# Optimization experiments

Measured on AMD Instinct MI355X. Metric: run time of the kernel, lower is better.

The kernel has to match this reference:

```python
import jax, jax.numpy as jnp
import numpy as np

EPS = 1e-20
K, STRIDE, PAD = 5, 2, 2
B, CIN, COUT, H, W = 4, 32, 32, 192, 192
HO = (H + 2 * PAD - K) // STRIDE + 1
WO = (W + 2 * PAD - K) // STRIDE + 1


def _patches(x, pad_value):
    # x: [B,C,H,W] -> [B,C,K*K,HO,WO]; same window layout as F.max_pool2d
    xp = jnp.pad(x, ((0, 0), (0, 0), (PAD, PAD), (PAD, PAD)), constant_values=pad_value)
    cols = [xp[:, :, dy:dy + STRIDE * HO:STRIDE, dx:dx + STRIDE * WO:STRIDE]
            for dy in range(K) for dx in range(K)]
    return jnp.stack(cols, axis=2)


def setup_inputs() -> dict:
    key = jax.random.key(0)
    ks = jax.random.split(key, 9)
    d = jax.random.uniform(ks[0], (B, CIN, H, W), jnp.float32, 0.05, 1.0)
    cd = jax.random.uniform(ks[1], (B, CIN, H, W), jnp.float32)
    s = jax.random.uniform(ks[2], (B, CIN, H, W), jnp.float32)
    cs = jax.random.uniform(ks[3], (B, CIN, H, W), jnp.float32)
    w_s_from_d = jax.random.normal(ks[4], (1, 1, 1, 1), jnp.float32) * 0.5
    w_prop = jax.random.normal(ks[5], (1, CIN, 1, 1), jnp.float32) * 0.5
    spatial_weight = jax.random.normal(ks[6], (CIN, 1, K, K), jnp.float32) * 0.5
    channel_weight = jax.random.normal(ks[7], (COUT, CIN, 1, 1), jnp.float32) * 0.5
    bias = jax.random.normal(ks[8], (1, COUT, 1, 1), jnp.float32) * 0.1
    return {"d": d, "cd": cd, "s": s, "cs": cs, "w_s_from_d": w_s_from_d,
            "w_prop": w_prop, "spatial_weight": spatial_weight,
            "channel_weight": channel_weight, "bias": bias}


def reference(d, cd, s, cs, w_s_from_d, w_prop, spatial_weight, channel_weight, bias):
    # EnforcePos reparameterization applied at forward time
    w_sfd = jax.nn.sigmoid(w_s_from_d)
    w_p = jax.nn.softplus(w_prop)
    sw = jax.nn.softplus(spatial_weight)   # [CIN,1,K,K] depthwise
    cw = jax.nn.softplus(channel_weight)   # [COUT,CIN,1,1]

    # max-pool argmax indices (torch pads with -inf), then gather d/cd at those indices
    j_max = jnp.argmax(_patches(d * cd, -jnp.inf), axis=2, keepdims=True)
    j_min = jnp.argmax(_patches(cd / (d + EPS), -jnp.inf), axis=2, keepdims=True)
    p_d = _patches(d, 0.0)
    p_cd = _patches(cd, 0.0)
    d_max = jnp.take_along_axis(p_d, j_max, axis=2)[:, :, 0]
    d_min = jnp.take_along_axis(p_d, j_min, axis=2)[:, :, 0]
    cd_max = jnp.take_along_axis(p_cd, j_max, axis=2)[:, :, 0]
    cd_min = jnp.take_along_axis(p_cd, j_min, axis=2)[:, :, 0]

    min_div_max = jnp.abs(d_min / (d_max + EPS))
    s_from_d = (1 - w_sfd) * min_div_max + w_sfd * min_div_max ** 2
    cs_from_d = cd_max * cd_min

    # stride > 1: no pre-propagation
    s_prop, cs_prop = s, cs

    dn = ('NCHW', 'OIHW', 'NCHW')
    def dwconv(x):  # depthwise 5x5, stride 2, pad 2
        return jax.lax.conv_general_dilated(
            x, sw, (STRIDE, STRIDE), [(PAD, PAD), (PAD, PAD)],
            feature_group_count=CIN, dimension_numbers=dn)

    nom = dwconv(cs_prop * s_prop)
    denom = dwconv(cs_prop)
    s_spatial = nom / (denom + EPS)
    cs_spatial = denom / (jnp.sum(sw) + EPS)

    cw2 = cw[:, :, 0, 0]  # [COUT,CIN], 1x1 conv == channel mixing
    nom = jnp.einsum('bihw,oi->bohw', cs_spatial * s_spatial, cw2)
    denom = jnp.einsum('bihw,oi->bohw', cs_spatial, cw2)
    s_out = nom / (denom + EPS)
    cs_out = denom / (jnp.sum(cw) + EPS)

    # stride > 1: merge pooled s_from_d afterwards
    s_out = (w_p * cs_out * s_out + cs_from_d * s_from_d) / (w_p * cs_out + cs_from_d + EPS)
    cs_out = (w_p * cs_out + cs_from_d) / (w_p + 1)

    s_out = s_out + bias
    s_out = jax.nn.sigmoid(s_out * 2 - 1) / 2 + 0.5
    return s_out, cs_out / (STRIDE * STRIDE)
```

## Files before the change

### kernel.cpp

```cpp
#include <hip/hip_runtime.h>

#define KK    5
#define PADV  2
#define NB    4
#define NC    32
#define NH    192
#define NW    192
#define NHO   96
#define NWO   96
#define NPX   (NHO * NWO)
#define NPLANE (NB * NC * NPX)
#define EPSF  1e-20f

__device__ __forceinline__ float softplusf(float x) {
    return fmaxf(x, 0.f) + log1pf(expf(-fabsf(x)));
}

#define TROWS 19
#define NJ    98
#define PLD2  100
#define K1T   768

__global__ __launch_bounds__(K1T, 6) void k1(
    const float* __restrict__ dg,
    const float* __restrict__ cdg,
    const float* __restrict__ sg,
    const float* __restrict__ csg,
    const float* __restrict__ wsfdg,
    const float* __restrict__ spwg,
    float* __restrict__ ws)
{
    __shared__ float2 pmv_e[TROWS][PLD2];
    __shared__ float2 pmv_o[TROWS][PLD2];
    __shared__ float2 csss_e[TROWS][PLD2];
    __shared__ float2 csss_o[TROWS][PLD2];
    __shared__ float sw_row[25];
    __shared__ float red[12];
    __shared__ float scal[2];

    const int t  = threadIdx.x;
    const int bx = blockIdx.x;
    const int c  = blockIdx.y;
    const int b  = blockIdx.z;

    float part = 0.f;
    for (int i = t; i < NC * 25; i += K1T) {
        float v = softplusf(spwg[i]);
        part += v;
        int cr = i - c * 25;
        if (cr >= 0 && cr < 25) sw_row[cr] = v;
    }
#pragma unroll
    for (int m = 32; m >= 1; m >>= 1) part += __shfl_xor(part, m, 64);
    if ((t & 63) == 0) red[t >> 6] = part;
    __syncthreads();
    if (t == 0) {
        float acc = 0.f;
#pragma unroll
        for (int i = 0; i < 12; i++) acc += red[i];
        scal[0] = acc;
        scal[1] = 1.f / (1.f + expf(-wsfdg[0]));
    }
    __syncthreads();

    const int gy0 = 16 * bx - 2;
    const size_t base = ((size_t)(b * NC) + c) * (NH * NW);
    const int ITEMS = TROWS * NJ;
#pragma unroll
    for (int it0 = 0; it0 < 3 * K1T; it0 += K1T) {
        const int it = it0 + t;
        if (it < ITEMS) {
            const int r  = it / NJ;
            const int j  = it - r * NJ;
            const int gy = gy0 + r;
            const int cc = 2 * j - 2;
            const bool ok = ((unsigned)gy < NH) && (j >= 1) && (j <= 96);
            float2 dv2 = make_float2(0.f, 0.f), cdv2 = dv2, sv2 = dv2, csv2 = dv2;
            if (ok) {
                const size_t idx = base + (size_t)gy * NW + cc;
                dv2  = *(const float2*)(dg  + idx);
                cdv2 = *(const float2*)(cdg + idx);
                sv2  = *(const float2*)(sg  + idx);
                csv2 = *(const float2*)(csg + idx);
            }
            float2 pe, po, ce, co;
            if (ok) {
                pe = make_float2(dv2.x * cdv2.x, cdv2.x / (dv2.x + EPSF));
                po = make_float2(dv2.y * cdv2.y, cdv2.y / (dv2.y + EPSF));
            } else {
                pe = make_float2(-INFINITY, -INFINITY);
                po = pe;
            }
            ce = make_float2(csv2.x, csv2.x * sv2.x);
            co = make_float2(csv2.y, csv2.y * sv2.y);
            pmv_e[r][j]  = pe;
            pmv_o[r][j]  = po;
            csss_e[r][j] = ce;
            csss_o[r][j] = co;
        }
    }
    __syncthreads();

    const int oyl = t / 96;
    const int ox  = t - oyl * 96;
    const int r0  = oyl * 2;

    float bm = -INFINITY, bv = -INFINITY;
    int   jm = 0, jv = 0;
    float nom = 0.f, den = 0.f;

#pragma unroll
    for (int dy = 0; dy < 5; dy++) {
        const int r = r0 + dy;
        const float w0 = sw_row[dy * 5 + 0];
        const float w1 = sw_row[dy * 5 + 1];
        const float w2 = sw_row[dy * 5 + 2];
        const float w3 = sw_row[dy * 5 + 3];
        const float w4 = sw_row[dy * 5 + 4];

        const float2 e0 = pmv_e[r][ox];
        const float2 o0 = pmv_o[r][ox];
        const float2 e1 = pmv_e[r][ox + 1];
        const float2 o1 = pmv_o[r][ox + 1];
        const float2 e2 = pmv_e[r][ox + 2];

        const float2 c0 = csss_e[r][ox];
        const float2 d1 = csss_o[r][ox];
        const float2 c1 = csss_e[r][ox + 1];
        const float2 d3 = csss_o[r][ox + 1];
        const float2 c2 = csss_e[r][ox + 2];

        if (e0.x > bm) { bm = e0.x; jm = r * 8 + 0; }
        if (e0.y > bv) { bv = e0.y; jv = r * 8 + 0; }
        if (o0.x > bm) { bm = o0.x; jm = r * 8 + 1; }
        if (o0.y > bv) { bv = o0.y; jv = r * 8 + 1; }
        if (e1.x > bm) { bm = e1.x; jm = r * 8 + 2; }
        if (e1.y > bv) { bv = e1.y; jv = r * 8 + 2; }
        if (o1.x > bm) { bm = o1.x; jm = r * 8 + 3; }
        if (o1.y > bv) { bv = o1.y; jv = r * 8 + 3; }
        if (e2.x > bm) { bm = e2.x; jm = r * 8 + 4; }
        if (e2.y > bv) { bv = e2.y; jv = r * 8 + 4; }

        nom += w0 * c0.y; den += w0 * c0.x;
        nom += w1 * d1.y; den += w1 * d1.x;
        nom += w2 * c1.y; den += w2 * c1.x;
        nom += w3 * d3.y; den += w3 * d3.x;
        nom += w4 * c2.y; den += w4 * c2.x;
    }

    const int rm = jm >> 3, dxm = jm & 7;
    const int rv = jv >> 3, dxv = jv & 7;
    const size_t im = base + (size_t)(gy0 + rm) * NW + (2 * ox - 2 + dxm);
    const size_t iv = base + (size_t)(gy0 + rv) * NW + (2 * ox - 2 + dxv);
    const float dmax = dg[im], cdmax = cdg[im];
    const float dmin = dg[iv], cdmin = cdg[iv];

    const float sumsw = scal[0];
    const float wsfd  = scal[1];
    const float mdm  = fabsf(dmin / (dmax + EPSF));
    const float sfd  = (1.f - wsfd) * mdm + wsfd * mdm * mdm;
    const float cfd  = cdmax * cdmin;
    const float ssp  = nom / (den + EPSF);
    const float cssp = den / (sumsw + EPSF);

    const int opx = (8 * bx + oyl) * NWO + ox;
    const size_t oidx = ((size_t)(b * NC) + c) * NPX + opx;
    ws[oidx]                       = cssp * ssp;
    ws[(size_t)NPLANE + oidx]      = cssp;
    ws[2 * (size_t)NPLANE + oidx]  = sfd;
    ws[3 * (size_t)NPLANE + oidx]  = cfd;
}

#define K2PX 32

__global__ __launch_bounds__(256, 8) void k2(
    const float* __restrict__ ws,
    const float* __restrict__ wpropg,
    const float* __restrict__ chwg,
    const float* __restrict__ biasg,
    float* __restrict__ out)
{
    __shared__ float cw_s[NC * NC];
    __shared__ float wp_s[NC];
    __shared__ float bias_s[NC];
    __shared__ float A_s[NC][K2PX + 1];
    __shared__ float B_s[NC][K2PX + 1];
    __shared__ float red[4];
    __shared__ float scal[1];

    const int t    = threadIdx.x;
    const int b    = blockIdx.y;
    const int px0  = blockIdx.x * K2PX;
    const int p    = t & (K2PX - 1);
    const int slot = t >> 5;

    float part = 0.f;
    for (int i = t; i < NC * NC; i += 256) {
        float v = softplusf(chwg[i]); cw_s[i] = v; part += v;
    }
    if (t < NC) { wp_s[t] = softplusf(wpropg[t]); bias_s[t] = biasg[t]; }
#pragma unroll
    for (int m = 32; m >= 1; m >>= 1) part += __shfl_xor(part, m, 64);
    if ((t & 63) == 0) red[t >> 6] = part;
    __syncthreads();
    if (t == 0) scal[0] = red[0] + red[1] + red[2] + red[3];

    const size_t bb = (size_t)b * NC * NPX;
#pragma unroll
    for (int idx = 0; idx < NC * K2PX; idx += 256) {
        const int i  = (idx + t) >> 5;
        const int pp = (idx + t) & (K2PX - 1);
        A_s[i][pp] = ws[bb + (size_t)i * NPX + px0 + pp];
        B_s[i][pp] = ws[(size_t)NPLANE + bb + (size_t)i * NPX + px0 + pp];
    }
    __syncthreads();

    const float sumcw = scal[0];
    const int px = px0 + p;

    float nom2[4], den2[4];
#pragma unroll
    for (int k = 0; k < 4; k++) { nom2[k] = 0.f; den2[k] = 0.f; }

#pragma unroll
    for (int i = 0; i < NC; i++) {
        const float a  = A_s[i][p];
        const float b2 = B_s[i][p];
#pragma unroll
        for (int k = 0; k < 4; k++) {
            const float w = cw_s[(slot + 8 * k) * NC + i];
            nom2[k] += w * a;
            den2[k] += w * b2;
        }
    }

#pragma unroll
    for (int k = 0; k < 4; k++) {
        const int o = slot + 8 * k;
        const size_t oidx = bb + (size_t)o * NPX + px;
        const float sfd = ws[2 * (size_t)NPLANE + oidx];
        const float cfd = ws[3 * (size_t)NPLANE + oidx];

        const float smix  = nom2[k] / (den2[k] + EPSF);
        const float csmix = den2[k] / (sumcw + EPSF);
        const float wp    = wp_s[o];

        float sout = (wp * csmix * smix + cfd * sfd) / (wp * csmix + cfd + EPSF);
        const float csout = (wp * csmix + cfd) / (wp + 1.f);

        sout += bias_s[o];
        sout = 1.f / (1.f + expf(-(sout * 2.f - 1.f))) * 0.5f + 0.5f;

        out[oidx]                  = sout;
        out[(size_t)NPLANE + oidx] = csout * 0.25f;
    }
}

#define TW    8
#define TH    4
#define TPP   33

__global__ __launch_bounds__(256, 4) void fused_kernel(
    const float* __restrict__ dg,
    const float* __restrict__ cdg,
    const float* __restrict__ sg,
    const float* __restrict__ csg,
    const float* __restrict__ wsfdg,
    const float* __restrict__ wpropg,
    const float* __restrict__ spwg,
    const float* __restrict__ chwg,
    const float* __restrict__ biasg,
    float* __restrict__ out)
{
    __shared__ float sw_s[NC * 25];
    __shared__ float cw_s[NC * NC];
    __shared__ float wp_s[NC];
    __shared__ float bias_s[NC];
    __shared__ float A_s[NC][TPP];
    __shared__ float B_s[NC][TPP];
    __shared__ float S_s[NC][TPP];
    __shared__ float C_s[NC][TPP];
    __shared__ float red[8];
    __shared__ float scal[3];

    const int t = threadIdx.x;
    const int b = blockIdx.z;
    const int tile_x = blockIdx.x * TW;
    const int tile_y = blockIdx.y * TH;

    float p_sw = 0.f, p_cw = 0.f;
    for (int i = t; i < NC * 25; i += 256) { float v = softplusf(spwg[i]); sw_s[i] = v; p_sw += v; }
    for (int i = t; i < NC * NC; i += 256) { float v = softplusf(chwg[i]); cw_s[i] = v; p_cw += v; }
    if (t < NC) { wp_s[t] = softplusf(wpropg[t]); bias_s[t] = biasg[t]; }
#pragma unroll
    for (int m = 32; m >= 1; m >>= 1) {
        p_sw += __shfl_xor(p_sw, m, 64);
        p_cw += __shfl_xor(p_cw, m, 64);
    }
    if ((t & 63) == 0) { red[(t >> 6) * 2] = p_sw; red[(t >> 6) * 2 + 1] = p_cw; }
    __syncthreads();
    if (t == 0) {
        scal[0] = red[0] + red[2] + red[4] + red[6];
        scal[1] = red[1] + red[3] + red[5] + red[7];
        scal[2] = 1.f / (1.f + expf(-wsfdg[0]));
    }
    __syncthreads();

    const float sumsw = scal[0];
    const float sumcw = scal[1];
    const float wsfd  = scal[2];

    const int c  = t >> 3;
    const int tr = (t >> 2) & 1;
    const int q  = t & 3;
    const int oy0 = tile_y + tr * 2;
    const int ox0 = tile_x + q * 2;
    const int cb = ox0 * 2 - 2;
    const int rb = oy0 * 2 - 2;
    const size_t base = ((size_t)(b * NC) + c) * NH * NW;
    const float* __restrict__ dp  = dg  + base;
    const float* __restrict__ cdp = cdg + base;
    const float* __restrict__ sp  = sg  + base;
    const float* __restrict__ csp = csg + base;

    bool slotok[4];
#pragma unroll
    for (int k = 0; k < 4; k++) slotok[k] = (cb + 2 * k >= 0) && (cb + 2 * k + 1 < NW);
    bool ciok[7];
#pragma unroll
    for (int ci = 0; ci < 7; ci++) ciok[ci] = ((unsigned)(cb + ci) < NW);

    float bm[2][2], dM[2][2], cM[2][2];
    float bn[2][2], dN[2][2], cN[2][2];
    float nom[2][2], den[2][2];
#pragma unroll
    for (int r = 0; r < 2; r++)
#pragma unroll
        for (int q2 = 0; q2 < 2; q2++) {
            bm[r][q2] = -INFINITY; bn[r][q2] = -INFINITY;
            dM[r][q2] = 0.f; cM[r][q2] = 0.f; dN[r][q2] = 0.f; cN[r][q2] = 0.f;
            nom[r][q2] = 0.f; den[r][q2] = 0.f;
        }

#pragma unroll
    for (int rr = 0; rr < 7; rr++) {
        const int iy = rb + rr;
        if ((unsigned)iy < NH) {
            const int roff = iy * NW + cb;
            float dv[8], cdv[8], sv[8], csv[8];
#pragma unroll
            for (int k = 0; k < 4; k++) {
                float2 vD, vCD, vS, vCS;
                if (slotok[k]) {
                    vD  = *(const float2*)(dp  + roff + 2 * k);
                    vCD = *(const float2*)(cdp + roff + 2 * k);
                    vS  = *(const float2*)(sp  + roff + 2 * k);
                    vCS = *(const float2*)(csp + roff + 2 * k);
                } else {
                    vD = make_float2(0.f, 0.f); vCD = vD; vS = vD; vCS = vD;
                }
                dv[2*k] = vD.x;  dv[2*k+1] = vD.y;
                cdv[2*k] = vCD.x; cdv[2*k+1] = vCD.y;
                sv[2*k] = vS.x;  sv[2*k+1] = vS.y;
                csv[2*k] = vCS.x; csv[2*k+1] = vCS.y;
            }
            float pm[7], pv[7];
#pragma unroll
            for (int ci = 0; ci < 7; ci++) {
                pm[ci] = dv[ci] * cdv[ci];
                pv[ci] = cdv[ci] / (dv[ci] + EPSF);
            }
#pragma unroll
            for (int r = 0; r < 2; r++) {
                const int dy = rr - 2 * r;
                if (dy >= 0 && dy <= 4) {
#pragma unroll
                    for (int dx = 0; dx < 5; dx++) {
                        const float w = sw_s[c * 25 + dy * 5 + dx];
#pragma unroll
                        for (int q2 = 0; q2 < 2; q2++) {
                            const int ci = 2 * q2 + dx;
                            if (ciok[ci]) {
                                if (pm[ci] > bm[r][q2]) { bm[r][q2] = pm[ci]; dM[r][q2] = dv[ci]; cM[r][q2] = cdv[ci]; }
                                if (pv[ci] > bn[r][q2]) { bn[r][q2] = pv[ci]; dN[r][q2] = dv[ci]; cN[r][q2] = cdv[ci]; }
                                nom[r][q2] += w * (csv[ci] * sv[ci]);
                                den[r][q2] += w * csv[ci];
                            }
                        }
                    }
                }
            }
        }
    }

#pragma unroll
    for (int r = 0; r < 2; r++)
#pragma unroll
        for (int q2 = 0; q2 < 2; q2++) {
            const float mdm  = fabsf(dN[r][q2] / (dM[r][q2] + EPSF));
            const float sfd  = (1.f - wsfd) * mdm + wsfd * mdm * mdm;
            const float cfd  = cM[r][q2] * cN[r][q2];
            const float ssp  = nom[r][q2] / (den[r][q2] + EPSF);
            const float cssp = den[r][q2] / (sumsw + EPSF);
            const int p = (tr * 2 + r) * TW + (q * 2 + q2);
            A_s[c][p] = cssp * ssp;
            B_s[c][p] = cssp;
            S_s[c][p] = sfd;
            C_s[c][p] = cfd;
        }
    __syncthreads();

    const int p  = t & 31;
    const int o0 = t >> 5;
    const int py = p >> 3;
    const int pxx = p & 7;
    const int opx = (tile_y + py) * NWO + tile_x + pxx;

    float nom2[4], den2[4];
#pragma unroll
    for (int k = 0; k < 4; k++) { nom2[k] = 0.f; den2[k] = 0.f; }

#pragma unroll
    for (int i = 0; i < NC; i++) {
        const float a  = A_s[i][p];
        const float b2 = B_s[i][p];
#pragma unroll
        for (int k = 0; k < 4; k++) {
            const float w = cw_s[(o0 + 8 * k) * NC + i];
            nom2[k] += w * a;
            den2[k] += w * b2;
        }
    }

#pragma unroll
    for (int k = 0; k < 4; k++) {
        const int o = o0 + 8 * k;
        const float smix  = nom2[k] / (den2[k] + EPSF);
        const float csmix = den2[k] / (sumcw + EPSF);
        const float wp    = wp_s[o];
        const float sfd   = S_s[o][p];
        const float cfd   = C_s[o][p];

        float sout = (wp * csmix * smix + cfd * sfd) / (wp * csmix + cfd + EPSF);
        const float csout = (wp * csmix + cfd) / (wp + 1.f);

        sout += bias_s[o];
        sout = 1.f / (1.f + expf(-(sout * 2.f - 1.f))) * 0.5f + 0.5f;

        const int oidx = ((b * NC) + o) * NPX + opx;
        out[oidx]          = sout;
        out[NPLANE + oidx] = csout * 0.25f;
    }
}

extern "C" void kernel_launch(void* const* d_in, const int* in_sizes, int n_in,
                              void* d_out, int out_size, void* d_ws, size_t ws_size,
                              hipStream_t stream) {
    const float* d     = (const float*)d_in[0];
    const float* cd    = (const float*)d_in[1];
    const float* s     = (const float*)d_in[2];
    const float* cs    = (const float*)d_in[3];
    const float* wsfd  = (const float*)d_in[4];
    const float* wprop = (const float*)d_in[5];
    const float* spw   = (const float*)d_in[6];
    const float* chw   = (const float*)d_in[7];
    const float* bias  = (const float*)d_in[8];
    float* out = (float*)d_out;

    const size_t need = (size_t)4 * NPLANE * sizeof(float);
    if (ws_size >= need) {
        float* ws = (float*)d_ws;
        k1<<<dim3(NHO / 8, NC, NB), K1T, 0, stream>>>(d, cd, s, cs, wsfd, spw, ws);
        k2<<<dim3(NPX / K2PX, NB), 256, 0, stream>>>(ws, wprop, chw, bias, out);
    } else {
        fused_kernel<<<dim3(NWO / TW, NHO / TH, NB), 256, 0, stream>>>(
            d, cd, s, cs, wsfd, wprop, spw, chw, bias, out);
    }
}
```

Measured before the change: 46.40 us.

## Recover pooled d/cd algebraically, pack workspace as float4, shrink k1 row tile

k1 no longer keeps argmax indices and re-reads d and cd from global memory. It carries the paired product and ratio values from the winning window elements and recovers d_min/d_max and cd_max*cd_min with sqrt of products. The four intermediate planes are written as one interleaved float4 per pixel instead of four separate planes. k2 reads that float4 once and stages the s_from_d and cs_from_d terms in shared memory. k1 now handles 6 output rows per 576-thread block instead of 8 per 768, and its launch-bounds occupancy hint rises from 6 to 7. The sqrt reconstruction drops the EPS terms and adds rounding error, which is a small accuracy risk.

```diff
diff --git a/kernel.cpp b/kernel.cpp
--- a/kernel.cpp
+++ b/kernel.cpp
@@ -16,26 +16,26 @@
     return fmaxf(x, 0.f) + log1pf(expf(-fabsf(x)));
 }
 
-#define TROWS 19
+#define TROWS 15
 #define NJ    98
 #define PLD2  100
-#define K1T   768
-
-__global__ __launch_bounds__(K1T, 6) void k1(
+#define K1T   576
+
+__global__ __launch_bounds__(K1T, 7) void k1(
     const float* __restrict__ dg,
     const float* __restrict__ cdg,
     const float* __restrict__ sg,
     const float* __restrict__ csg,
     const float* __restrict__ wsfdg,
     const float* __restrict__ spwg,
-    float* __restrict__ ws)
+    float4* __restrict__ ws4)
 {
     __shared__ float2 pmv_e[TROWS][PLD2];
     __shared__ float2 pmv_o[TROWS][PLD2];
     __shared__ float2 csss_e[TROWS][PLD2];
     __shared__ float2 csss_o[TROWS][PLD2];
     __shared__ float sw_row[25];
-    __shared__ float red[12];
+    __shared__ float red[9];
     __shared__ float scal[2];
 
     const int t  = threadIdx.x;
@@ -57,13 +57,13 @@
     if (t == 0) {
         float acc = 0.f;
 #pragma unroll
-        for (int i = 0; i < 12; i++) acc += red[i];
+        for (int i = 0; i < 9; i++) acc += red[i];
         scal[0] = acc;
         scal[1] = 1.f / (1.f + expf(-wsfdg[0]));
     }
     __syncthreads();
 
-    const int gy0 = 16 * bx - 2;
+    const int gy0 = 12 * bx - 2;
     const size_t base = ((size_t)(b * NC) + c) * (NH * NW);
     const int ITEMS = TROWS * NJ;
 #pragma unroll
@@ -83,7 +83,7 @@
                 sv2  = *(const float2*)(sg  + idx);
                 csv2 = *(const float2*)(csg + idx);
             }
-            float2 pe, po, ce, co;
+            float2 pe, po;
             if (ok) {
                 pe = make_float2(dv2.x * cdv2.x, cdv2.x / (dv2.x + EPSF));
                 po = make_float2(dv2.y * cdv2.y, cdv2.y / (dv2.y + EPSF));
@@ -91,12 +91,10 @@
                 pe = make_float2(-INFINITY, -INFINITY);
                 po = pe;
             }
-            ce = make_float2(csv2.x, csv2.x * sv2.x);
-            co = make_float2(csv2.y, csv2.y * sv2.y);
             pmv_e[r][j]  = pe;
             pmv_o[r][j]  = po;
-            csss_e[r][j] = ce;
-            csss_o[r][j] = co;
+            csss_e[r][j] = make_float2(csv2.x, csv2.x * sv2.x);
+            csss_o[r][j] = make_float2(csv2.y, csv2.y * sv2.y);
         }
     }
     __syncthreads();
@@ -106,7 +104,7 @@
     const int r0  = oyl * 2;
 
     float bm = -INFINITY, bv = -INFINITY;
-    int   jm = 0, jv = 0;
+    float pvm = 0.f, pmn = 0.f;
     float nom = 0.f, den = 0.f;
 
 #pragma unroll
@@ -130,16 +128,16 @@
         const float2 d3 = csss_o[r][ox + 1];
         const float2 c2 = csss_e[r][ox + 2];
 
-        if (e0.x > bm) { bm = e0.x; jm = r * 8 + 0; }
-        if (e0.y > bv) { bv = e0.y; jv = r * 8 + 0; }
-        if (o0.x > bm) { bm = o0.x; jm = r * 8 + 1; }
-        if (o0.y > bv) { bv = o0.y; jv = r * 8 + 1; }
-        if (e1.x > bm) { bm = e1.x; jm = r * 8 + 2; }
-        if (e1.y > bv) { bv = e1.y; jv = r * 8 + 2; }
-        if (o1.x > bm) { bm = o1.x; jm = r * 8 + 3; }
-        if (o1.y > bv) { bv = o1.y; jv = r * 8 + 3; }
-        if (e2.x > bm) { bm = e2.x; jm = r * 8 + 4; }
-        if (e2.y > bv) { bv = e2.y; jv = r * 8 + 4; }
+        if (e0.x > bm) { bm = e0.x; pvm = e0.y; }
+        if (e0.y > bv) { bv = e0.y; pmn = e0.x; }
+        if (o0.x > bm) { bm = o0.x; pvm = o0.y; }
+        if (o0.y > bv) { bv = o0.y; pmn = o0.x; }
+        if (e1.x > bm) { bm = e1.x; pvm = e1.y; }
+        if (e1.y > bv) { bv = e1.y; pmn = e1.x; }
+        if (o1.x > bm) { bm = o1.x; pvm = o1.y; }
+        if (o1.y > bv) { bv = o1.y; pmn = o1.x; }
+        if (e2.x > bm) { bm = e2.x; pvm = e2.y; }
+        if (e2.y > bv) { bv = e2.y; pmn = e2.x; }
 
         nom += w0 * c0.y; den += w0 * c0.x;
         nom += w1 * d1.y; den += w1 * d1.x;
@@ -148,33 +146,26 @@
         nom += w4 * c2.y; den += w4 * c2.x;
     }
 
-    const int rm = jm >> 3, dxm = jm & 7;
-    const int rv = jv >> 3, dxv = jv & 7;
-    const size_t im = base + (size_t)(gy0 + rm) * NW + (2 * ox - 2 + dxm);
-    const size_t iv = base + (size_t)(gy0 + rv) * NW + (2 * ox - 2 + dxv);
-    const float dmax = dg[im], cdmax = cdg[im];
-    const float dmin = dg[iv], cdmin = cdg[iv];
+    const float t1 = pmn * pvm;
+    const float t2 = bv * bm;
+    const float mdm = fabsf(sqrtf(t1 / t2));
+    const float cfd = sqrtf(t1 * t2);
 
     const float sumsw = scal[0];
     const float wsfd  = scal[1];
-    const float mdm  = fabsf(dmin / (dmax + EPSF));
     const float sfd  = (1.f - wsfd) * mdm + wsfd * mdm * mdm;
-    const float cfd  = cdmax * cdmin;
     const float ssp  = nom / (den + EPSF);
     const float cssp = den / (sumsw + EPSF);
 
-    const int opx = (8 * bx + oyl) * NWO + ox;
+    const int opx = (6 * bx + oyl) * NWO + ox;
     const size_t oidx = ((size_t)(b * NC) + c) * NPX + opx;
-    ws[oidx]                       = cssp * ssp;
-    ws[(size_t)NPLANE + oidx]      = cssp;
-    ws[2 * (size_t)NPLANE + oidx]  = sfd;
-    ws[3 * (size_t)NPLANE + oidx]  = cfd;
+    ws4[oidx] = make_float4(cssp * ssp, cssp, sfd, cfd);
 }
 
 #define K2PX 32
 
 __global__ __launch_bounds__(256, 8) void k2(
-    const float* __restrict__ ws,
+    const float4* __restrict__ ws4,
     const float* __restrict__ wpropg,
     const float* __restrict__ chwg,
     const float* __restrict__ biasg,
@@ -185,6 +176,8 @@
     __shared__ float bias_s[NC];
     __shared__ float A_s[NC][K2PX + 1];
     __shared__ float B_s[NC][K2PX + 1];
+    __shared__ float S_s[NC][K2PX + 1];
+    __shared__ float C_s[NC][K2PX + 1];
     __shared__ float red[4];
     __shared__ float scal[1];
 
@@ -210,8 +203,11 @@
     for (int idx = 0; idx < NC * K2PX; idx += 256) {
         const int i  = (idx + t) >> 5;
         const int pp = (idx + t) & (K2PX - 1);
-        A_s[i][pp] = ws[bb + (size_t)i * NPX + px0 + pp];
-        B_s[i][pp] = ws[(size_t)NPLANE + bb + (size_t)i * NPX + px0 + pp];
+        const float4 q = ws4[bb + (size_t)i * NPX + px0 + pp];
+        A_s[i][pp] = q.x;
+        B_s[i][pp] = q.y;
+        S_s[i][pp] = q.z;
+        C_s[i][pp] = q.w;
     }
     __syncthreads();
 
@@ -237,9 +233,8 @@
 #pragma unroll
     for (int k = 0; k < 4; k++) {
         const int o = slot + 8 * k;
-        const size_t oidx = bb + (size_t)o * NPX + px;
-        const float sfd = ws[2 * (size_t)NPLANE + oidx];
-        const float cfd = ws[3 * (size_t)NPLANE + oidx];
+        const float sfd = S_s[o][p];
+        const float cfd = C_s[o][p];
 
         const float smix  = nom2[k] / (den2[k] + EPSF);
         const float csmix = den2[k] / (sumcw + EPSF);
@@ -251,6 +246,7 @@
         sout += bias_s[o];
         sout = 1.f / (1.f + expf(-(sout * 2.f - 1.f))) * 0.5f + 0.5f;
 
+        const size_t oidx = bb + (size_t)o * NPX + px;
         out[oidx]                  = sout;
         out[(size_t)NPLANE + oidx] = csout * 0.25f;
     }
@@ -469,9 +465,9 @@
 
     const size_t need = (size_t)4 * NPLANE * sizeof(float);
     if (ws_size >= need) {
-        float* ws = (float*)d_ws;
-        k1<<<dim3(NHO / 8, NC, NB), K1T, 0, stream>>>(d, cd, s, cs, wsfd, spw, ws);
-        k2<<<dim3(NPX / K2PX, NB), 256, 0, stream>>>(ws, wprop, chw, bias, out);
+        float4* ws4 = (float4*)d_ws;
+        k1<<<dim3(NHO / 6, NC, NB), K1T, 0, stream>>>(d, cd, s, cs, wsfd, spw, ws4);
+        k2<<<dim3(NPX / K2PX, NB), 256, 0, stream>>>(ws4, wprop, chw, bias, out);
     } else {
         fused_kernel<<<dim3(NWO / TW, NHO / TH, NB), 256, 0, stream>>>(
             d, cd, s, cs, wsfd, wprop, spw, chw, bias, out);
```

After: 49.88 us. 7.5% more time.
